# Optimization experiments

Measured on AMD Instinct MI355X. Metric: run time of the kernel, lower is better.

Reference implementation:

```python
import jax, jax.numpy as jnp
import numpy as np

MARGIN = 0.8  # TripletMarginMiner(margin=0.8, type_of_triplets='semihard')
Z_DIM = 512
N_CONCEPT = 64
NUM_TASK, NUM_SHOT, NUM_WAY = 16, 5, 5


def _triplet_indices(num_shot, num_way):
    # labels = torch.arange(num_way).repeat(num_shot) -> tile pattern
    labels = np.tile(np.arange(num_way), num_shot)
    N = labels.shape[0]
    same = labels[:, None] == labels[None, :]
    pos = same & ~np.eye(N, dtype=bool)          # a != p, same label
    neg = ~same                                  # different label
    a, p, n = np.nonzero(pos[:, :, None] & neg[:, None, :])  # all candidate triplets
    return jnp.asarray(a), jnp.asarray(p), jnp.asarray(n)


def setup_inputs() -> dict:
    key = jax.random.key(0)
    ks = jax.random.split(key, 12)
    d = Z_DIM
    s = lambda fan: 1.0 / np.sqrt(fan)
    inp = {
        'input_data': jax.random.normal(ks[0], (NUM_TASK, NUM_SHOT, NUM_WAY, d), jnp.float32),
        # proj_inner: Linear(3d -> 2d), ReLU, Linear(2d -> d)
        'W1': jax.random.normal(ks[1], (3 * d, 2 * d), jnp.float32) * s(3 * d),
        'b1': jnp.zeros((2 * d,), jnp.float32),
        'W2': jax.random.normal(ks[2], (2 * d, d), jnp.float32) * s(2 * d),
        'b2': jnp.zeros((d,), jnp.float32),
        # proj_outer: Linear(d -> 2d), ReLU, Linear(2d -> d)
        'W3': jax.random.normal(ks[3], (d, 2 * d), jnp.float32) * s(d),
        'b3': jnp.zeros((2 * d,), jnp.float32),
        'W4': jax.random.normal(ks[4], (2 * d, d), jnp.float32) * s(2 * d),
        'b4': jnp.zeros((d,), jnp.float32),
        # cls: Linear(d -> n_concept)
        'Wc': jax.random.normal(ks[5], (d, N_CONCEPT), jnp.float32) * s(d),
        'bc': jnp.zeros((N_CONCEPT,), jnp.float32),
    }
    return inp


def reference(input_data, W1, b1, W2, b2, W3, b3, W4, b4, Wc, bc):
    num_task, num_shot, num_way, d = input_data.shape
    x = input_data.reshape(num_task, num_shot * num_way, d)  # [K, N, d]
    a, p, n = _triplet_indices(num_shot, num_way)            # fixed triplet set [T]

    # --- semihard mining (no grad; binary mask so no grad path anyway) ---
    # LpDistance default: normalize embeddings, then L2 distance
    xn = x / jnp.linalg.norm(x, axis=-1, keepdims=True)
    sq = jnp.sum(xn * xn, axis=-1)                           # [K, N]
    D2 = sq[:, :, None] + sq[:, None, :] - 2.0 * jnp.einsum('kid,kjd->kij', xn, xn)
    D = jnp.sqrt(jnp.clip(D2, 0.0))                          # [K, N, N]
    tm = D[:, a, n] - D[:, a, p]                             # an_dist - ap_dist, [K, T]
    mask = ((tm > 0.0) & (tm <= MARGIN)).astype(x.dtype)     # semihard: 0 < margin <= 0.8

    # --- gather triplet embeddings (unnormalized), concat [x_a, x_p, x_n] ---
    feat = jnp.concatenate([x[:, a], x[:, p], x[:, n]], axis=-1)  # [K, T, 3d]

    # proj_inner then masked sum over mined triplets per task
    h = jax.nn.relu(feat @ W1 + b1) @ W2 + b2                # [K, T, d]
    pooled = jnp.einsum('ktd,kt->kd', h, mask)               # [K, d]

    o = jax.nn.relu(pooled @ W3 + b3) @ W4 + b4              # [K, d]
    score = o @ Wc + bc                                      # [K, n_concept]
    return jax.nn.softmax(score, axis=-1)
```

## Files before the change

kernel.cpp:

```cpp
#include <hip/hip_runtime.h>
#include <math.h>

#define NT 16
#define NR 25
#define DZ 512
#define D2Z 1024
#define NC 64

typedef short bf16x8 __attribute__((ext_vector_type(8)));
typedef float f32x4  __attribute__((ext_vector_type(4)));

#define TP  76
#define XSP 520
#define CP  68

static __device__ inline unsigned short f2bf(float v) {
    union { float f; unsigned u; } x; x.f = v;
    unsigned r = x.u + 0x7fffu + ((x.u >> 16) & 1u);
    return (unsigned short)(r >> 16);
}
static __device__ inline float bf2f(unsigned short h) {
    union { float f; unsigned u; } x; x.u = ((unsigned)h) << 16; return x.f;
}

__global__ __launch_bounds__(256) void k_prep(
    const float* __restrict__ x, const float* __restrict__ W1,
    unsigned short* __restrict__ W1h, unsigned short* __restrict__ W1l,
    float* __restrict__ Dm)
{
    __shared__ unsigned short th[64 * TP], tl[64 * TP];
    int vb = blockIdx.x;
    int tid = threadIdx.x;

    if (vb < 384) {
        int r0 = (vb % 24) * 64;
        int j0 = (vb / 24) * 64;
        int c  = r0 >> 9;
        int rb = r0 & 511;

        #pragma unroll
        for (int it = 0; it < 4; it++) {
            int rl = (tid >> 4) + it * 16;
            int jj = (tid & 15) * 4;
            float4 v = *(const float4*)(W1 + (size_t)(r0 + rl) * D2Z + j0 + jj);
            unsigned short h0 = f2bf(v.x), h1 = f2bf(v.y), h2 = f2bf(v.z), h3 = f2bf(v.w);
            th[rl * TP + jj + 0] = h0; tl[rl * TP + jj + 0] = f2bf(v.x - bf2f(h0));
            th[rl * TP + jj + 1] = h1; tl[rl * TP + jj + 1] = f2bf(v.y - bf2f(h1));
            th[rl * TP + jj + 2] = h2; tl[rl * TP + jj + 2] = f2bf(v.z - bf2f(h2));
            th[rl * TP + jj + 3] = h3; tl[rl * TP + jj + 3] = f2bf(v.w - bf2f(h3));
        }
        __syncthreads();

        #pragma unroll
        for (int it = 0; it < 4; it++) {
            int jl = (tid >> 4) + it * 16;
            int r4 = (tid & 15) * 4;
            ushort4 hv = make_ushort4(th[(r4+0)*TP + jl], th[(r4+1)*TP + jl],
                                      th[(r4+2)*TP + jl], th[(r4+3)*TP + jl]);
            ushort4 lv = make_ushort4(tl[(r4+0)*TP + jl], tl[(r4+1)*TP + jl],
                                      tl[(r4+2)*TP + jl], tl[(r4+3)*TP + jl]);
            size_t dst = ((size_t)c * D2Z + j0 + jl) * DZ + rb + r4;
            *(ushort4*)(W1h + dst) = hv;
            *(ushort4*)(W1l + dst) = lv;
        }
    } else {
        int i = vb - 384;
        int k = i & 15, a = i >> 4;
        int lane = tid & 63;
        int w    = tid >> 6;
        const float* xk = x + (size_t)k * NR * DZ;

        const float4* xap = (const float4*)(xk + a * DZ);
        float4 a0 = xap[lane];
        float4 a1 = xap[lane + 64];

        float sa = a0.x*a0.x + a0.y*a0.y + a0.z*a0.z + a0.w*a0.w
                 + a1.x*a1.x + a1.y*a1.y + a1.z*a1.z + a1.w*a1.w;
        #pragma unroll
        for (int off = 32; off; off >>= 1) sa += __shfl_xor(sa, off);
        float inva = 1.0f / sqrtf(sa);
        a0.x *= inva; a0.y *= inva; a0.z *= inva; a0.w *= inva;
        a1.x *= inva; a1.y *= inva; a1.z *= inva; a1.w *= inva;
        float sqa = a0.x*a0.x + a0.y*a0.y + a0.z*a0.z + a0.w*a0.w
                  + a1.x*a1.x + a1.y*a1.y + a1.z*a1.z + a1.w*a1.w;
        #pragma unroll
        for (int off = 32; off; off >>= 1) sqa += __shfl_xor(sqa, off);

        for (int j = w; j < NR; j += 4) {
            const float4* xjp = (const float4*)(xk + j * DZ);
            float4 j0 = xjp[lane];
            float4 j1 = xjp[lane + 64];
            float sj = j0.x*j0.x + j0.y*j0.y + j0.z*j0.z + j0.w*j0.w
                     + j1.x*j1.x + j1.y*j1.y + j1.z*j1.z + j1.w*j1.w;
            #pragma unroll
            for (int off = 32; off; off >>= 1) sj += __shfl_xor(sj, off);
            float invj = 1.0f / sqrtf(sj);
            j0.x *= invj; j0.y *= invj; j0.z *= invj; j0.w *= invj;
            j1.x *= invj; j1.y *= invj; j1.z *= invj; j1.w *= invj;

            float sqj = j0.x*j0.x + j0.y*j0.y + j0.z*j0.z + j0.w*j0.w
                      + j1.x*j1.x + j1.y*j1.y + j1.z*j1.z + j1.w*j1.w;
            float dij = a0.x*j0.x + a0.y*j0.y + a0.z*j0.z + a0.w*j0.w
                      + a1.x*j1.x + a1.y*j1.y + a1.z*j1.z + a1.w*j1.w;
            #pragma unroll
            for (int off = 32; off; off >>= 1) {
                sqj += __shfl_xor(sqj, off);
                dij += __shfl_xor(dij, off);
            }
            float d2 = sqa + sqj - 2.0f * dij;
            float d  = sqrtf(fmaxf(d2, 0.0f));
            if (lane == 0) Dm[((size_t)k * NR + a) * NR + j] = d;
        }
    }
}

__global__ __launch_bounds__(512) void k_fused(
    const float* __restrict__ x,
    const unsigned short* __restrict__ W1h, const unsigned short* __restrict__ W1l,
    const float* __restrict__ b1, const float* __restrict__ Dm,
    float* __restrict__ G, float* __restrict__ cnt)
{
    __shared__ unsigned short xs_h[25 * XSP], xs_l[25 * XSP];
    __shared__ float Ct[2][75 * CP];
    __shared__ float Dm_s[NR * NR];
    __shared__ float red[8][64];
    __shared__ float cred[4];

    int bid = blockIdx.x;
    int k  = bid >> 4;
    int jt = bid & 15;
    int j0 = jt * 64;

    int tid  = threadIdx.x;
    int lane = tid & 63;
    int w    = tid >> 6;
    int g    = w & 3;
    int kh   = w >> 2;
    int q    = lane >> 4;
    int ln16 = lane & 15;

    for (int idx = tid; idx < NR * NR; idx += 512)
        Dm_s[idx] = Dm[(size_t)k * NR * NR + idx];

    for (int gi = tid; gi < NR * 64; gi += 512) {
        int row = gi >> 6;
        int c8  = (gi & 63) * 8;
        const float* xp = x + ((size_t)k * NR + row) * DZ + c8;
        float4 v0 = *(const float4*)(xp);
        float4 v1 = *(const float4*)(xp + 4);
        unsigned short h;
        ushort4 ha, hb, la, lb;
        h = f2bf(v0.x); ha.x = h; la.x = f2bf(v0.x - bf2f(h));
        h = f2bf(v0.y); ha.y = h; la.y = f2bf(v0.y - bf2f(h));
        h = f2bf(v0.z); ha.z = h; la.z = f2bf(v0.z - bf2f(h));
        h = f2bf(v0.w); ha.w = h; la.w = f2bf(v0.w - bf2f(h));
        h = f2bf(v1.x); hb.x = h; lb.x = f2bf(v1.x - bf2f(h));
        h = f2bf(v1.y); hb.y = h; lb.y = f2bf(v1.y - bf2f(h));
        h = f2bf(v1.z); hb.z = h; lb.z = f2bf(v1.z - bf2f(h));
        h = f2bf(v1.w); hb.w = h; lb.w = f2bf(v1.w - bf2f(h));
        *(ushort4*)&xs_h[row * XSP + c8]     = ha;
        *(ushort4*)&xs_h[row * XSP + c8 + 4] = hb;
        *(ushort4*)&xs_l[row * XSP + c8]     = la;
        *(ushort4*)&xs_l[row * XSP + c8 + 4] = lb;
    }
    __syncthreads();

    if (jt == 0 && tid < 256) {
        float cntv = 0.0f;
        for (int idx = tid; idx < 2000; idx += 256) {
            int a   = idx / 80;
            int rem = idx - a * 80;
            int mi  = rem / 20;
            int nn  = rem - mi * 20;
            int qa = a % 5, mdiv = a / 5;
            int m = mi + (mi >= mdiv);
            int p = qa + 5 * m;
            int ng = nn >> 2, o = nn & 3;
            int n = ng * 5 + o + (o >= qa);
            float tm = Dm_s[a * NR + n] - Dm_s[a * NR + p];
            cntv += ((tm > 0.0f) && (tm <= 0.8f)) ? 1.0f : 0.0f;
        }
        #pragma unroll
        for (int off = 32; off; off >>= 1) cntv += __shfl_xor(cntv, off);
        if (lane == 0) cred[w] = cntv;
    }

    int rowA1 = 16 + ln16;
    if (rowA1 > 24) rowA1 = 24;

    const unsigned short* wb_h = W1h + ((size_t)j0 + g * 16 + ln16) * DZ + q * 8;
    const unsigned short* wb_l = W1l + ((size_t)j0 + g * 16 + ln16) * DZ + q * 8;

    for (int c = 0; c < 3; c++) {
        f32x4 acc0 = (f32x4){0.f,0.f,0.f,0.f};
        f32x4 acc1 = (f32x4){0.f,0.f,0.f,0.f};
        const unsigned short* wch = wb_h + (size_t)c * D2Z * DZ;
        const unsigned short* wcl = wb_l + (size_t)c * D2Z * DZ;

        #pragma unroll
        for (int kc2 = 0; kc2 < 8; kc2++) {
            int kc  = kh * 8 + kc2;
            int kog = kc * 32 + q * 8;
            bf16x8 b_h = *(const bf16x8*)(wch + kc * 32);
            bf16x8 b_l = *(const bf16x8*)(wcl + kc * 32);
            bf16x8 a0h = *(const bf16x8*)&xs_h[ln16 * XSP + kog];
            bf16x8 a0l = *(const bf16x8*)&xs_l[ln16 * XSP + kog];
            bf16x8 a1h = *(const bf16x8*)&xs_h[rowA1 * XSP + kog];
            bf16x8 a1l = *(const bf16x8*)&xs_l[rowA1 * XSP + kog];
            acc0 = __builtin_amdgcn_mfma_f32_16x16x32_bf16(a0h, b_h, acc0, 0, 0, 0);
            acc0 = __builtin_amdgcn_mfma_f32_16x16x32_bf16(a0h, b_l, acc0, 0, 0, 0);
            acc0 = __builtin_amdgcn_mfma_f32_16x16x32_bf16(a0l, b_h, acc0, 0, 0, 0);
            acc1 = __builtin_amdgcn_mfma_f32_16x16x32_bf16(a1h, b_h, acc1, 0, 0, 0);
            acc1 = __builtin_amdgcn_mfma_f32_16x16x32_bf16(a1h, b_l, acc1, 0, 0, 0);
            acc1 = __builtin_amdgcn_mfma_f32_16x16x32_bf16(a1l, b_h, acc1, 0, 0, 0);
        }

        int col = g * 16 + ln16;
        #pragma unroll
        for (int r = 0; r < 4; r++) {
            int r0 = q * 4 + r;
            Ct[kh][(c * 25 + r0) * CP + col] = acc0[r];
            int r1 = 16 + q * 4 + r;
            if (r1 < 25) Ct[kh][(c * 25 + r1) * CP + col] = acc1[r];
        }
    }
    __syncthreads();

    if (jt == 0 && tid == 0)
        cnt[k] = cred[0] + cred[1] + cred[2] + cred[3];

    int j  = tid & 63;
    int h  = (tid >> 6) & 3;
    int ag = tid >> 8;
    float b1v = b1[j0 + j];

    float a3v[NR];
    #pragma unroll
    for (int i = 0; i < NR; i++)
        a3v[i] = Ct[0][(50 + i) * CP + j] + Ct[1][(50 + i) * CP + j];

    float acc = 0.0f;
    #define ACC_BODY(a) { \
        const int qa = (a) % 5, mdiv = (a) / 5; \
        int m = h + (h >= mdiv); \
        int p = qa + 5 * m; \
        float a1v = Ct[0][(a) * CP + j] + Ct[1][(a) * CP + j]; \
        float a2v = Ct[0][(25 + p) * CP + j] + Ct[1][(25 + p) * CP + j]; \
        float dap = Dm_s[(a) * NR + p]; \
        float s = a1v + a2v + b1v; \
        _Pragma("unroll") \
        for (int ng = 0; ng < 5; ng++) { \
            _Pragma("unroll") \
            for (int o = 0; o < 4; o++) { \
                int n = ng * 5 + o + (o >= qa); \
                float tm = Dm_s[(a) * NR + n] - dap; \
                bool sel = (tm > 0.0f) && (tm <= 0.8f); \
                float pre = fmaxf(s + a3v[n], 0.0f); \
                acc = fmaf(sel ? 1.0f : 0.0f, pre, acc); \
            } \
        } }
    if (ag == 0) {
        #pragma unroll
        for (int a = 0; a < 13; a++) ACC_BODY(a)
    } else {
        #pragma unroll
        for (int a = 13; a < 25; a++) ACC_BODY(a)
    }
    #undef ACC_BODY

    red[tid >> 6][j] = acc;
    __syncthreads();
    if (tid < 64) {
        float s = 0.0f;
        #pragma unroll
        for (int r = 0; r < 8; r++) s += red[r][tid];
        G[(size_t)k * D2Z + j0 + tid] = s;
    }
}


__global__ __launch_bounds__(256) void kA(const float* __restrict__ G,
                                          const float* __restrict__ W2,
                                          float* __restrict__ pp)
{
    __shared__ float GsT[256 * 16];
    __shared__ float red2[4][16][64];
    int ct = blockIdx.x & 7, jq = blockIdx.x >> 3;
    int tid = threadIdx.x;

    for (int idx = tid; idx < 4096; idx += 256) {
        int t = idx & 15, jj = idx >> 4;
        GsT[jj * 16 + t] = G[(size_t)t * D2Z + jq * 256 + jj];
    }
    __syncthreads();

    int cg = tid & 63, sub = tid >> 6;
    int col = ct * 64 + cg;
    float acc[16];
    #pragma unroll
    for (int t = 0; t < 16; t++) acc[t] = 0.0f;

    for (int jj = 0; jj < 64; jj++) {
        int jr = sub * 64 + jj;
        float wv = W2[(size_t)(jq * 256 + jr) * DZ + col];
        const float4* gp = (const float4*)&GsT[jr * 16];
        float4 g0 = gp[0], g1 = gp[1], g2 = gp[2], g3 = gp[3];
        acc[0]  = fmaf(g0.x, wv, acc[0]);  acc[1]  = fmaf(g0.y, wv, acc[1]);
        acc[2]  = fmaf(g0.z, wv, acc[2]);  acc[3]  = fmaf(g0.w, wv, acc[3]);
        acc[4]  = fmaf(g1.x, wv, acc[4]);  acc[5]  = fmaf(g1.y, wv, acc[5]);
        acc[6]  = fmaf(g1.z, wv, acc[6]);  acc[7]  = fmaf(g1.w, wv, acc[7]);
        acc[8]  = fmaf(g2.x, wv, acc[8]);  acc[9]  = fmaf(g2.y, wv, acc[9]);
        acc[10] = fmaf(g2.z, wv, acc[10]); acc[11] = fmaf(g2.w, wv, acc[11]);
        acc[12] = fmaf(g3.x, wv, acc[12]); acc[13] = fmaf(g3.y, wv, acc[13]);
        acc[14] = fmaf(g3.z, wv, acc[14]); acc[15] = fmaf(g3.w, wv, acc[15]);
    }
    #pragma unroll
    for (int t = 0; t < 16; t++) red2[sub][t][cg] = acc[t];
    __syncthreads();
    for (int r = 0; r < 4; r++) {
        int oi = tid + r * 256;
        int t = oi >> 6, c2 = oi & 63;
        float s = red2[0][t][c2] + red2[1][t][c2] + red2[2][t][c2] + red2[3][t][c2];
        pp[(size_t)jq * 8192 + t * DZ + ct * 64 + c2] = s;
    }
}

__global__ __launch_bounds__(256) void kB(const float* __restrict__ pp,
                                          const float* __restrict__ cnt,
                                          const float* __restrict__ b2,
                                          const float* __restrict__ W3,
                                          float* __restrict__ up)
{
    __shared__ float PsT[128 * 16];
    __shared__ float red2[4][16][64];
    int ct = blockIdx.x & 15, cq = blockIdx.x >> 4;
    int tid = threadIdx.x;

    for (int idx = tid; idx < 2048; idx += 256) {
        int t = idx & 15, cl = idx >> 4;
        int c = cq * 128 + cl;
        float v = pp[t * DZ + c]           + pp[8192  + t * DZ + c]
                + pp[16384 + t * DZ + c]   + pp[24576 + t * DZ + c]
                + cnt[t] * b2[c];
        PsT[cl * 16 + t] = v;
    }
    __syncthreads();

    int cg = tid & 63, sub = tid >> 6;
    int col = ct * 64 + cg;
    float acc[16];
    #pragma unroll
    for (int t = 0; t < 16; t++) acc[t] = 0.0f;

    for (int cl = 0; cl < 32; cl++) {
        int cr = sub * 32 + cl;
        float wv = W3[(size_t)(cq * 128 + cr) * D2Z + col];
        const float4* gp = (const float4*)&PsT[cr * 16];
        float4 g0 = gp[0], g1 = gp[1], g2 = gp[2], g3 = gp[3];
        acc[0]  = fmaf(g0.x, wv, acc[0]);  acc[1]  = fmaf(g0.y, wv, acc[1]);
        acc[2]  = fmaf(g0.z, wv, acc[2]);  acc[3]  = fmaf(g0.w, wv, acc[3]);
        acc[4]  = fmaf(g1.x, wv, acc[4]);  acc[5]  = fmaf(g1.y, wv, acc[5]);
        acc[6]  = fmaf(g1.z, wv, acc[6]);  acc[7]  = fmaf(g1.w, wv, acc[7]);
        acc[8]  = fmaf(g2.x, wv, acc[8]);  acc[9]  = fmaf(g2.y, wv, acc[9]);
        acc[10] = fmaf(g2.z, wv, acc[10]); acc[11] = fmaf(g2.w, wv, acc[11]);
        acc[12] = fmaf(g3.x, wv, acc[12]); acc[13] = fmaf(g3.y, wv, acc[13]);
        acc[14] = fmaf(g3.z, wv, acc[14]); acc[15] = fmaf(g3.w, wv, acc[15]);
    }
    #pragma unroll
    for (int t = 0; t < 16; t++) red2[sub][t][cg] = acc[t];
    __syncthreads();
    for (int r = 0; r < 4; r++) {
        int oi = tid + r * 256;
        int t = oi >> 6, c2 = oi & 63;
        float s = red2[0][t][c2] + red2[1][t][c2] + red2[2][t][c2] + red2[3][t][c2];
        up[(size_t)cq * 16384 + t * D2Z + ct * 64 + c2] = s;
    }
}

__global__ __launch_bounds__(256) void kC(const float* __restrict__ up,
                                          const float* __restrict__ b3,
                                          const float* __restrict__ W4,
                                          float* __restrict__ op)
{
    __shared__ float UsT[256 * 16];
    __shared__ float red2[4][16][64];
    int ct = blockIdx.x & 7, sq = blockIdx.x >> 3;
    int tid = threadIdx.x;

    for (int idx = tid; idx < 4096; idx += 256) {
        int t = idx & 15, sl = idx >> 4;
        int s = sq * 256 + sl;
        float v = up[t * D2Z + s]           + up[16384 + t * D2Z + s]
                + up[32768 + t * D2Z + s]   + up[49152 + t * D2Z + s]
                + b3[s];
        UsT[sl * 16 + t] = fmaxf(v, 0.0f);
    }
    __syncthreads();

    int cg = tid & 63, sub = tid >> 6;
    int col = ct * 64 + cg;
    float acc[16];
    #pragma unroll
    for (int t = 0; t < 16; t++) acc[t] = 0.0f;

    for (int sl = 0; sl < 64; sl++) {
        int sr = sub * 64 + sl;
        float wv = W4[(size_t)(sq * 256 + sr) * DZ + col];
        const float4* gp = (const float4*)&UsT[sr * 16];
        float4 g0 = gp[0], g1 = gp[1], g2 = gp[2], g3 = gp[3];
        acc[0]  = fmaf(g0.x, wv, acc[0]);  acc[1]  = fmaf(g0.y, wv, acc[1]);
        acc[2]  = fmaf(g0.z, wv, acc[2]);  acc[3]  = fmaf(g0.w, wv, acc[3]);
        acc[4]  = fmaf(g1.x, wv, acc[4]);  acc[5]  = fmaf(g1.y, wv, acc[5]);
        acc[6]  = fmaf(g1.z, wv, acc[6]);  acc[7]  = fmaf(g1.w, wv, acc[7]);
        acc[8]  = fmaf(g2.x, wv, acc[8]);  acc[9]  = fmaf(g2.y, wv, acc[9]);
        acc[10] = fmaf(g2.z, wv, acc[10]); acc[11] = fmaf(g2.w, wv, acc[11]);
        acc[12] = fmaf(g3.x, wv, acc[12]); acc[13] = fmaf(g3.y, wv, acc[13]);
        acc[14] = fmaf(g3.z, wv, acc[14]); acc[15] = fmaf(g3.w, wv, acc[15]);
    }
    #pragma unroll
    for (int t = 0; t < 16; t++) red2[sub][t][cg] = acc[t];
    __syncthreads();
    for (int r = 0; r < 4; r++) {
        int oi = tid + r * 256;
        int t = oi >> 6, c2 = oi & 63;
        float s = red2[0][t][c2] + red2[1][t][c2] + red2[2][t][c2] + red2[3][t][c2];
        op[(size_t)sq * 8192 + t * DZ + ct * 64 + c2] = s;
    }
}

__global__ __launch_bounds__(256) void kD(const float* __restrict__ op,
                                          const float* __restrict__ b4,
                                          const float* __restrict__ Wc,
                                          const float* __restrict__ bc,
                                          float* __restrict__ out)
{
    __shared__ float Os[DZ];
    __shared__ float tmp[4][64];
    int k = blockIdx.x;
    int tid = threadIdx.x;

    for (int c = tid; c < DZ; c += 256)
        Os[c] = op[k * DZ + c]           + op[8192  + k * DZ + c]
              + op[16384 + k * DZ + c]   + op[24576 + k * DZ + c]
              + b4[c];
    __syncthreads();

    int oc = tid & 63, seg = tid >> 6;
    float a0 = 0.f, a1 = 0.f, a2 = 0.f, a3 = 0.f;
    int r0 = seg * 128;
    #pragma unroll 4
    for (int rr = r0; rr < r0 + 128; rr += 4) {
        a0 = fmaf(Os[rr+0], Wc[(size_t)(rr+0) * NC + oc], a0);
        a1 = fmaf(Os[rr+1], Wc[(size_t)(rr+1) * NC + oc], a1);
        a2 = fmaf(Os[rr+2], Wc[(size_t)(rr+2) * NC + oc], a2);
        a3 = fmaf(Os[rr+3], Wc[(size_t)(rr+3) * NC + oc], a3);
    }
    tmp[seg][oc] = (a0 + a1) + (a2 + a3);
    __syncthreads();
    if (tid < 64) {
        float sc = bc[tid] + tmp[0][tid] + tmp[1][tid] + tmp[2][tid] + tmp[3][tid];
        float m = sc;
        #pragma unroll
        for (int off = 32; off; off >>= 1) m = fmaxf(m, __shfl_xor(m, off));
        float e = expf(sc - m);
        float ss = e;
        #pragma unroll
        for (int off = 32; off; off >>= 1) ss += __shfl_xor(ss, off);
        out[k * NC + tid] = e / ss;
    }
}

extern "C" void kernel_launch(void* const* d_in, const int* in_sizes, int n_in,
                              void* d_out, int out_size, void* d_ws, size_t ws_size,
                              hipStream_t stream)
{
    const float* x  = (const float*)d_in[0];
    const float* W1 = (const float*)d_in[1];
    const float* b1 = (const float*)d_in[2];
    const float* W2 = (const float*)d_in[3];
    const float* b2 = (const float*)d_in[4];
    const float* W3 = (const float*)d_in[5];
    const float* b3 = (const float*)d_in[6];
    const float* W4 = (const float*)d_in[7];
    const float* b4 = (const float*)d_in[8];
    const float* Wc = (const float*)d_in[9];
    const float* bc = (const float*)d_in[10];
    float* out = (float*)d_out;

    float* ws   = (float*)d_ws;
    float* Dm   = ws;
    float* cnt  = ws + 10016;
    float* G    = ws + 10032;
    float* pp   = ws + 26416;
    float* up   = ws + 59184;
    float* op   = ws + 124720;
    unsigned short* W1h = (unsigned short*)(ws + 157488);
    unsigned short* W1l = W1h + 3 * D2Z * DZ;

    k_prep <<<784,          256, 0, stream>>>(x, W1, W1h, W1l, Dm);
    k_fused<<<256,          512, 0, stream>>>(x, W1h, W1l, b1, Dm, G, cnt);
    kA     <<<32,           256, 0, stream>>>(G, W2, pp);
    kB     <<<64,           256, 0, stream>>>(pp, cnt, b2, W3, up);
    kC     <<<32,           256, 0, stream>>>(up, b3, W4, op);
    kD     <<<NT,           256, 0, stream>>>(op, b4, Wc, bc, out);
}
```

Baseline: 150.4 us.

## Widen split-K parallelism in fused GEMM and tail MLP kernels

The fused W1 kernel moves to 1024 threads, splitting the K reduction four ways instead of two and spreading the anchor loop over four groups. The W2/W3/W4 kernels (kA, kB, kC) get a finer split-K with 128 blocks each, and the consumers sum 16 or 8 partials instead of 4. Workspace offsets grow to hold the extra partial buffers. The aim is to fill more CUs on the small tail GEMMs, at the cost of more partial-sum traffic, more LDS, and higher register pressure under the 1024-thread launch bound.

```diff
diff --git a/kernel.cpp b/kernel.cpp
--- a/kernel.cpp
+++ b/kernel.cpp
@@ -114,16 +114,16 @@
     }
 }
 
-__global__ __launch_bounds__(512) void k_fused(
+__global__ __launch_bounds__(1024) void k_fused(
     const float* __restrict__ x,
     const unsigned short* __restrict__ W1h, const unsigned short* __restrict__ W1l,
     const float* __restrict__ b1, const float* __restrict__ Dm,
     float* __restrict__ G, float* __restrict__ cnt)
 {
     __shared__ unsigned short xs_h[25 * XSP], xs_l[25 * XSP];
-    __shared__ float Ct[2][75 * CP];
+    __shared__ float Ct[4][75 * CP];
     __shared__ float Dm_s[NR * NR];
-    __shared__ float red[8][64];
+    __shared__ float red[16][64];
     __shared__ float cred[4];
 
     int bid = blockIdx.x;
@@ -139,10 +139,10 @@
     int q    = lane >> 4;
     int ln16 = lane & 15;
 
-    for (int idx = tid; idx < NR * NR; idx += 512)
+    for (int idx = tid; idx < NR * NR; idx += 1024)
         Dm_s[idx] = Dm[(size_t)k * NR * NR + idx];
 
-    for (int gi = tid; gi < NR * 64; gi += 512) {
+    for (int gi = tid; gi < NR * 64; gi += 1024) {
         int row = gi >> 6;
         int c8  = (gi & 63) * 8;
         const float* xp = x + ((size_t)k * NR + row) * DZ + c8;
@@ -198,8 +198,8 @@
         const unsigned short* wcl = wb_l + (size_t)c * D2Z * DZ;
 
         #pragma unroll
-        for (int kc2 = 0; kc2 < 8; kc2++) {
-            int kc  = kh * 8 + kc2;
+        for (int kc2 = 0; kc2 < 4; kc2++) {
+            int kc  = kh * 4 + kc2;
             int kog = kc * 32 + q * 8;
             bf16x8 b_h = *(const bf16x8*)(wch + kc * 32);
             bf16x8 b_l = *(const bf16x8*)(wcl + kc * 32);
@@ -237,15 +237,18 @@
     float a3v[NR];
     #pragma unroll
     for (int i = 0; i < NR; i++)
-        a3v[i] = Ct[0][(50 + i) * CP + j] + Ct[1][(50 + i) * CP + j];
+        a3v[i] = Ct[0][(50 + i) * CP + j] + Ct[1][(50 + i) * CP + j]
+               + Ct[2][(50 + i) * CP + j] + Ct[3][(50 + i) * CP + j];
 
     float acc = 0.0f;
     #define ACC_BODY(a) { \
         const int qa = (a) % 5, mdiv = (a) / 5; \
         int m = h + (h >= mdiv); \
         int p = qa + 5 * m; \
-        float a1v = Ct[0][(a) * CP + j] + Ct[1][(a) * CP + j]; \
-        float a2v = Ct[0][(25 + p) * CP + j] + Ct[1][(25 + p) * CP + j]; \
+        float a1v = Ct[0][(a) * CP + j] + Ct[1][(a) * CP + j] \
+                  + Ct[2][(a) * CP + j] + Ct[3][(a) * CP + j]; \
+        float a2v = Ct[0][(25 + p) * CP + j] + Ct[1][(25 + p) * CP + j] \
+                  + Ct[2][(25 + p) * CP + j] + Ct[3][(25 + p) * CP + j]; \
         float dap = Dm_s[(a) * NR + p]; \
         float s = a1v + a2v + b1v; \
         _Pragma("unroll") \
@@ -261,10 +264,16 @@
         } }
     if (ag == 0) {
         #pragma unroll
-        for (int a = 0; a < 13; a++) ACC_BODY(a)
+        for (int a = 0; a < 7; a++) ACC_BODY(a)
+    } else if (ag == 1) {
+        #pragma unroll
+        for (int a = 7; a < 13; a++) ACC_BODY(a)
+    } else if (ag == 2) {
+        #pragma unroll
+        for (int a = 13; a < 19; a++) ACC_BODY(a)
     } else {
         #pragma unroll
-        for (int a = 13; a < 25; a++) ACC_BODY(a)
+        for (int a = 19; a < 25; a++) ACC_BODY(a)
     }
     #undef ACC_BODY
 
@@ -273,7 +282,7 @@
     if (tid < 64) {
         float s = 0.0f;
         #pragma unroll
-        for (int r = 0; r < 8; r++) s += red[r][tid];
+        for (int r = 0; r < 16; r++) s += red[r][tid];
         G[(size_t)k * D2Z + j0 + tid] = s;
     }
 }
@@ -283,14 +292,14 @@
                                           const float* __restrict__ W2,
                                           float* __restrict__ pp)
 {
-    __shared__ float GsT[256 * 16];
+    __shared__ float GsT[64 * 16];
     __shared__ float red2[4][16][64];
     int ct = blockIdx.x & 7, jq = blockIdx.x >> 3;
     int tid = threadIdx.x;
 
-    for (int idx = tid; idx < 4096; idx += 256) {
+    for (int idx = tid; idx < 1024; idx += 256) {
         int t = idx & 15, jj = idx >> 4;
-        GsT[jj * 16 + t] = G[(size_t)t * D2Z + jq * 256 + jj];
+        GsT[jj * 16 + t] = G[(size_t)t * D2Z + jq * 64 + jj];
     }
     __syncthreads();
 
@@ -300,9 +309,9 @@
     #pragma unroll
     for (int t = 0; t < 16; t++) acc[t] = 0.0f;
 
-    for (int jj = 0; jj < 64; jj++) {
-        int jr = sub * 64 + jj;
-        float wv = W2[(size_t)(jq * 256 + jr) * DZ + col];
+    for (int jj = 0; jj < 16; jj++) {
+        int jr = sub * 16 + jj;
+        float wv = W2[(size_t)(jq * 64 + jr) * DZ + col];
         const float4* gp = (const float4*)&GsT[jr * 16];
         float4 g0 = gp[0], g1 = gp[1], g2 = gp[2], g3 = gp[3];
         acc[0]  = fmaf(g0.x, wv, acc[0]);  acc[1]  = fmaf(g0.y, wv, acc[1]);
@@ -331,17 +340,18 @@
                                           const float* __restrict__ W3,
                                           float* __restrict__ up)
 {
-    __shared__ float PsT[128 * 16];
+    __shared__ float PsT[64 * 16];
     __shared__ float red2[4][16][64];
     int ct = blockIdx.x & 15, cq = blockIdx.x >> 4;
     int tid = threadIdx.x;
 
-    for (int idx = tid; idx < 2048; idx += 256) {
+    for (int idx = tid; idx < 1024; idx += 256) {
         int t = idx & 15, cl = idx >> 4;
-        int c = cq * 128 + cl;
-        float v = pp[t * DZ + c]           + pp[8192  + t * DZ + c]
-                + pp[16384 + t * DZ + c]   + pp[24576 + t * DZ + c]
-                + cnt[t] * b2[c];
+        int c = cq * 64 + cl;
+        float v = cnt[t] * b2[c];
+        #pragma unroll
+        for (int sl = 0; sl < 16; sl++)
+            v += pp[(size_t)sl * 8192 + t * DZ + c];
         PsT[cl * 16 + t] = v;
     }
     __syncthreads();
@@ -352,9 +362,9 @@
     #pragma unroll
     for (int t = 0; t < 16; t++) acc[t] = 0.0f;
 
-    for (int cl = 0; cl < 32; cl++) {
-        int cr = sub * 32 + cl;
-        float wv = W3[(size_t)(cq * 128 + cr) * D2Z + col];
+    for (int cl = 0; cl < 16; cl++) {
+        int cr = sub * 16 + cl;
+        float wv = W3[(size_t)(cq * 64 + cr) * D2Z + col];
         const float4* gp = (const float4*)&PsT[cr * 16];
         float4 g0 = gp[0], g1 = gp[1], g2 = gp[2], g3 = gp[3];
         acc[0]  = fmaf(g0.x, wv, acc[0]);  acc[1]  = fmaf(g0.y, wv, acc[1]);
@@ -382,17 +392,18 @@
                                           const float* __restrict__ W4,
                                           float* __restrict__ op)
 {
-    __shared__ float UsT[256 * 16];
+    __shared__ float UsT[64 * 16];
     __shared__ float red2[4][16][64];
     int ct = blockIdx.x & 7, sq = blockIdx.x >> 3;
     int tid = threadIdx.x;
 
-    for (int idx = tid; idx < 4096; idx += 256) {
+    for (int idx = tid; idx < 1024; idx += 256) {
         int t = idx & 15, sl = idx >> 4;
-        int s = sq * 256 + sl;
-        float v = up[t * D2Z + s]           + up[16384 + t * D2Z + s]
-                + up[32768 + t * D2Z + s]   + up[49152 + t * D2Z + s]
-                + b3[s];
+        int s = sq * 64 + sl;
+        float v = b3[s];
+        #pragma unroll
+        for (int c8 = 0; c8 < 8; c8++)
+            v += up[(size_t)c8 * 16384 + t * D2Z + s];
         UsT[sl * 16 + t] = fmaxf(v, 0.0f);
     }
     __syncthreads();
@@ -403,9 +414,9 @@
     #pragma unroll
     for (int t = 0; t < 16; t++) acc[t] = 0.0f;
 
-    for (int sl = 0; sl < 64; sl++) {
-        int sr = sub * 64 + sl;
-        float wv = W4[(size_t)(sq * 256 + sr) * DZ + col];
+    for (int sl = 0; sl < 16; sl++) {
+        int sr = sub * 16 + sl;
+        float wv = W4[(size_t)(sq * 64 + sr) * DZ + col];
         const float4* gp = (const float4*)&UsT[sr * 16];
         float4 g0 = gp[0], g1 = gp[1], g2 = gp[2], g3 = gp[3];
         acc[0]  = fmaf(g0.x, wv, acc[0]);  acc[1]  = fmaf(g0.y, wv, acc[1]);
@@ -439,10 +450,13 @@
     int k = blockIdx.x;
     int tid = threadIdx.x;
 
-    for (int c = tid; c < DZ; c += 256)
-        Os[c] = op[k * DZ + c]           + op[8192  + k * DZ + c]
-              + op[16384 + k * DZ + c]   + op[24576 + k * DZ + c]
-              + b4[c];
+    for (int c = tid; c < DZ; c += 256) {
+        float v = b4[c];
+        #pragma unroll
+        for (int sl = 0; sl < 16; sl++)
+            v += op[(size_t)sl * 8192 + k * DZ + c];
+        Os[c] = v;
+    }
     __syncthreads();
 
     int oc = tid & 63, seg = tid >> 6;
@@ -492,15 +506,15 @@
     float* cnt  = ws + 10016;
     float* G    = ws + 10032;
     float* pp   = ws + 26416;
-    float* up   = ws + 59184;
-    float* op   = ws + 124720;
-    unsigned short* W1h = (unsigned short*)(ws + 157488);
+    float* up   = ws + 157488;
+    float* op   = ws + 288560;
+    unsigned short* W1h = (unsigned short*)(ws + 419632);
     unsigned short* W1l = W1h + 3 * D2Z * DZ;
 
-    k_prep <<<784,          256, 0, stream>>>(x, W1, W1h, W1l, Dm);
-    k_fused<<<256,          512, 0, stream>>>(x, W1h, W1l, b1, Dm, G, cnt);
-    kA     <<<32,           256, 0, stream>>>(G, W2, pp);
-    kB     <<<64,           256, 0, stream>>>(pp, cnt, b2, W3, up);
-    kC     <<<32,           256, 0, stream>>>(up, b3, W4, op);
-    kD     <<<NT,           256, 0, stream>>>(op, b4, Wc, bc, out);
-}
+    k_prep <<<784,  256, 0, stream>>>(x, W1, W1h, W1l, Dm);
+    k_fused<<<256, 1024, 0, stream>>>(x, W1h, W1l, b1, Dm, G, cnt);
+    kA     <<<128,  256, 0, stream>>>(G, W2, pp);
+    kB     <<<128,  256, 0, stream>>>(pp, cnt, b2, W3, up);
+    kC     <<<128,  256, 0, stream>>>(up, b3, W4, op);
+    kD     <<<NT,   256, 0, stream>>>(op, b4, Wc, bc, out);
+}
```

New measurement: 138.3 us. 8.1% less time.
